# Kernel tuning notes

Hardware: AMD Instinct MI355X
Metric: run time of the kernel (lower is better)

## Reference

```python
import jax, jax.numpy as jnp
import numpy as np

# ---- module constants (from GranuleCellLayer.__init__) ----
N_MOSSY = 4096
EXPANSION = 4.0
N_GRANULE = int(N_MOSSY * EXPANSION)  # 16384
SPARSITY = 0.03
K = int(N_GRANULE * SPARSITY)  # 491
DT_MS = 1.0
# ConductanceLIFConfig(v_threshold=-50, v_reset=-65, tau_mem=5, tau_E=2.5, tau_I=6)
V_TH = -50.0
V_RESET = -65.0
TAU_MEM = 5.0
E_LEAK = -65.0   # assumed == v_reset
E_EXC = 0.0      # standard excitatory reversal potential
W_SPARSITY = 0.05  # WeightInitializer.sparse_random sparsity


def setup_inputs() -> dict:
    key = jax.random.key(0)
    k1, k2, k3, k4 = jax.random.split(key, 4)
    mossy_fiber_spikes = (jax.random.uniform(k1, (N_MOSSY,)) < 0.2).astype(jnp.float32)
    # Per-synapse STP efficacy in (0, 1], shape [n_mossy, n_granule].
    mf_efficacy = jax.random.uniform(k2, (N_MOSSY, N_GRANULE), dtype=jnp.float32)
    mask = (jax.random.uniform(k3, (N_GRANULE, N_MOSSY)) < W_SPARSITY).astype(jnp.float32)
    W = mask * jax.random.uniform(k4, (N_GRANULE, N_MOSSY), dtype=jnp.float32)
    return {"mossy_fiber_spikes": mossy_fiber_spikes, "mf_efficacy": mf_efficacy, "W": W}


def _lif_step(g_exc):
    """Single conductance-LIF Euler step from rest (v=v_reset, g_I=0)."""
    v0 = V_RESET
    # dv = dt/tau_mem * ( (E_L - v) + g_E*(E_E - v) )   (no inhibitory input)
    dv = (DT_MS / TAU_MEM) * ((E_LEAK - v0) + g_exc * (E_EXC - v0))
    v = v0 + dv
    return v >= V_TH  # bool spikes [n_granule]


def reference(mossy_fiber_spikes, mf_efficacy, W):
    # effective_weights = W * mf_efficacy.T ; g_exc = effective_weights @ spikes
    g_exc = jnp.einsum('gm,mg,m->g', W, mf_efficacy, mossy_fiber_spikes)  # [n_granule]
    spikes = _lif_step(g_exc)  # bool [n_granule]
    n_spiking = jnp.sum(spikes.astype(jnp.int32))
    # winner-take-all: keep top-k by excitatory conductance among spiking cells
    masked = jnp.where(spikes, g_exc, -jnp.inf)
    _, top_idx = jax.lax.top_k(masked, K)
    sparse_spikes = jnp.zeros((N_GRANULE,), dtype=bool).at[top_idx].set(True)
    out = jnp.where(n_spiking > K, sparse_spikes, spikes)
    return out
```

## Files before the change

### kernel.cpp

```cpp
#include <hip/hip_runtime.h>

#define N_MOSSY   4096
#define N_GRANULE 16384
#define K_TOP     491
#define M_SPLIT   16
#define M_PER     (N_MOSSY / M_SPLIT)
#define G_BLOCKS  (N_GRANULE / 256)

__global__ __launch_bounds__(256) void gexc_partial(
    const float* __restrict__ spikes,
    const float* __restrict__ eff,
    const float* __restrict__ W,
    float* __restrict__ partial)
{
    __shared__ int s_act[M_PER];
    __shared__ int s_cnt[4];
    __shared__ int s_off[5];

    const int tid  = threadIdx.x;
    const int lane = tid & 63;
    const int wv   = tid >> 6;
    const int mb   = blockIdx.x;
    const int gb   = blockIdx.y;
    const int ms   = mb * M_PER;

    const int m    = ms + wv * 64 + lane;
    const bool p   = spikes[m] > 0.0f;
    const unsigned long long mk = __ballot(p);
    const int pre  = __popcll(mk & ((1ull << lane) - 1ull));
    if (lane == 0) s_cnt[wv] = __popcll(mk);
    __syncthreads();
    if (tid == 0) {
        int o = 0;
        for (int c = 0; c < 4; ++c) { s_off[c] = o; o += s_cnt[c]; }
        s_off[4] = o;
    }
    __syncthreads();
    if (p) s_act[s_off[wv] + pre] = m;
    __syncthreads();
    const int nact = s_off[4];

    const int g = gb * 256 + tid;
    const float* __restrict__ wrow = W + (size_t)g * N_MOSSY;

    float acc = 0.0f;
    int j = 0;
    for (; j + 4 <= nact; j += 4) {
        const int m0 = s_act[j + 0], m1 = s_act[j + 1];
        const int m2 = s_act[j + 2], m3 = s_act[j + 3];
        const float w0 = wrow[m0], w1 = wrow[m1], w2 = wrow[m2], w3 = wrow[m3];
        const float e0 = eff[(size_t)m0 * N_GRANULE + g];
        const float e1 = eff[(size_t)m1 * N_GRANULE + g];
        const float e2 = eff[(size_t)m2 * N_GRANULE + g];
        const float e3 = eff[(size_t)m3 * N_GRANULE + g];
        acc += w0 * e0; acc += w1 * e1; acc += w2 * e2; acc += w3 * e3;
    }
    for (; j < nact; ++j) {
        const int m0 = s_act[j];
        acc += wrow[m0] * eff[(size_t)m0 * N_GRANULE + g];
    }
    partial[(size_t)mb * N_GRANULE + g] = acc;
}

#define NB   2048
#define BIN0 7680
#define CAP  2048

__global__ __launch_bounds__(1024) void reduce_select(
    const float* __restrict__ partial,
    int* __restrict__ out)
{
    __shared__ int s_hist[NB];
    __shared__ int s_scan[1024];
    __shared__ unsigned int s_cbits[CAP];
    __shared__ int s_cidx[CAP];
    __shared__ int s_ccnt;
    __shared__ int s_nspk;
    __shared__ int s_B;
    __shared__ int s_need;

    const int t = threadIdx.x;

    float gx[16];
    #pragma unroll
    for (int i = 0; i < 16; ++i) {
        const int g = i * 1024 + t;
        float a = 0.0f;
        #pragma unroll
        for (int s = 0; s < M_SPLIT; ++s)
            a += partial[(size_t)s * N_GRANULE + g];
        gx[i] = a;
    }

    unsigned int ubits[16];
    int spkmask = 0;
    int myspk = 0;
    #pragma unroll
    for (int i = 0; i < 16; ++i) {
        const float dv = 0.2f * (0.0f + gx[i] * 65.0f);
        const float v  = -65.0f + dv;
        const bool s   = (v >= -50.0f);
        if (s) { spkmask |= (1 << i); ++myspk; }
        ubits[i] = __float_as_uint(gx[i]);
    }

    if (t == 0) { s_ccnt = 0; s_nspk = 0; s_B = -1; s_need = 0; }
    for (int b = t; b < NB; b += 1024) s_hist[b] = 0;
    __syncthreads();

    atomicAdd(&s_nspk, myspk);
    #pragma unroll
    for (int i = 0; i < 16; ++i) {
        if ((spkmask >> i) & 1) {
            int b = (int)(ubits[i] >> 17) - BIN0;
            b = b < 0 ? 0 : (b >= NB ? NB - 1 : b);
            atomicAdd(&s_hist[b], 1);
        }
    }
    __syncthreads();

    const int nspk = s_nspk;

    if (nspk > K_TOP) {
        s_scan[t] = s_hist[2 * t] + s_hist[2 * t + 1];
        __syncthreads();
        for (int off = 1; off < 1024; off <<= 1) {
            const int v = (t + off < 1024) ? s_scan[t + off] : 0;
            __syncthreads();
            s_scan[t] += v;
            __syncthreads();
        }
        const int suf0 = s_scan[t];
        const int suf1 = s_scan[t] - s_hist[2 * t];
        if (suf0 >= K_TOP) atomicMax(&s_B, 2 * t);
        if (suf1 >= K_TOP) atomicMax(&s_B, 2 * t + 1);
        __syncthreads();
        const int B = s_B;
        if (t == 0) {
            const int sufB = s_scan[B >> 1] - ((B & 1) ? s_hist[B & ~1] : 0);
            s_need = K_TOP - (sufB - s_hist[B]);
        }
        __syncthreads();
        const int need = s_need;

        #pragma unroll
        for (int i = 0; i < 16; ++i) {
            if ((spkmask >> i) & 1) {
                int b = (int)(ubits[i] >> 17) - BIN0;
                b = b < 0 ? 0 : (b >= NB ? NB - 1 : b);
                if (b == B) {
                    const int pos = atomicAdd(&s_ccnt, 1);
                    if (pos < CAP) {
                        s_cbits[pos] = ubits[i];
                        s_cidx[pos]  = i * 1024 + t;
                    }
                }
            }
        }
        __syncthreads();
        int C = s_ccnt; if (C > CAP) C = CAP;

        #pragma unroll
        for (int i = 0; i < 16; ++i) {
            const int g = i * 1024 + t;
            bool sel = false;
            if ((spkmask >> i) & 1) {
                int b = (int)(ubits[i] >> 17) - BIN0;
                b = b < 0 ? 0 : (b >= NB ? NB - 1 : b);
                if (b > B) {
                    sel = true;
                } else if (b == B) {
                    int rank = 0;
                    for (int j = 0; j < C; ++j) {
                        const unsigned int cb = s_cbits[j];
                        const int ci = s_cidx[j];
                        if (cb > ubits[i] || (cb == ubits[i] && ci < g)) ++rank;
                    }
                    sel = (rank < need);
                }
            }
            out[g] = sel ? 1 : 0;
        }
    } else {
        #pragma unroll
        for (int i = 0; i < 16; ++i) {
            const int g = i * 1024 + t;
            out[g] = ((spkmask >> i) & 1) ? 1 : 0;
        }
    }
}

extern "C" void kernel_launch(void* const* d_in, const int* in_sizes, int n_in,
                              void* d_out, int out_size, void* d_ws, size_t ws_size,
                              hipStream_t stream) {
    const float* spikes = (const float*)d_in[0];
    const float* eff    = (const float*)d_in[1];
    const float* W      = (const float*)d_in[2];
    int* out       = (int*)d_out;
    float* partial = (float*)d_ws;

    gexc_partial<<<dim3(M_SPLIT, G_BLOCKS), 256, 0, stream>>>(spikes, eff, W, partial);
    reduce_select<<<1, 1024, 0, stream>>>(partial, out);
}
```

Measured before the change: 588.4 us.

## Stage W tiles via coalesced LDS transpose and parallelize reduction across blocks

After: 524.4 us. 1.12x faster.

```diff
diff --git a/kernel.cpp b/kernel.cpp
--- a/kernel.cpp
+++ b/kernel.cpp
@@ -4,15 +4,30 @@
 #define N_GRANULE 16384
 #define K_TOP     491
 #define M_SPLIT   16
-#define M_PER     (N_MOSSY / M_SPLIT)
-#define G_BLOCKS  (N_GRANULE / 256)
+#define M_PER     256
+#define G_BLOCKS  64
+#define CH        32
+#define NCH       (M_PER / CH)
+#define LDS_PAD   257
+
+#define NB   2048
+#define BIN0 7680
+#define CAP  2048
+
+#define WS_PARTIAL 0
+#define WS_UBITS   (M_SPLIT * N_GRANULE)
+#define WS_HIST    (WS_UBITS + N_GRANULE)
+#define WS_NSPK    (WS_HIST + NB)
 
 __global__ __launch_bounds__(256) void gexc_partial(
     const float* __restrict__ spikes,
     const float* __restrict__ eff,
     const float* __restrict__ W,
-    float* __restrict__ partial)
+    float* __restrict__ partial,
+    int* __restrict__ hist,
+    int* __restrict__ nspk)
 {
+    __shared__ float wl[CH][LDS_PAD];
     __shared__ int s_act[M_PER];
     __shared__ int s_cnt[4];
     __shared__ int s_off[5];
@@ -24,8 +39,13 @@
     const int gb   = blockIdx.y;
     const int ms   = mb * M_PER;
 
-    const int m    = ms + wv * 64 + lane;
-    const bool p   = spikes[m] > 0.0f;
+    if (mb == 0) {
+        if (gb < 8) hist[gb * 256 + tid] = 0;
+        else if (gb == 8 && tid == 0) *nspk = 0;
+    }
+
+    const int m0   = ms + wv * 64 + lane;
+    const bool p   = spikes[m0] > 0.0f;
     const unsigned long long mk = __ballot(p);
     const int pre  = __popcll(mk & ((1ull << lane) - 1ull));
     if (lane == 0) s_cnt[wv] = __popcll(mk);
@@ -36,38 +56,68 @@
         s_off[4] = o;
     }
     __syncthreads();
-    if (p) s_act[s_off[wv] + pre] = m;
+    if (p) s_act[s_off[wv] + pre] = m0;
     __syncthreads();
     const int nact = s_off[4];
 
     const int g = gb * 256 + tid;
-    const float* __restrict__ wrow = W + (size_t)g * N_MOSSY;
 
     float acc = 0.0f;
     int j = 0;
-    for (; j + 4 <= nact; j += 4) {
-        const int m0 = s_act[j + 0], m1 = s_act[j + 1];
-        const int m2 = s_act[j + 2], m3 = s_act[j + 3];
-        const float w0 = wrow[m0], w1 = wrow[m1], w2 = wrow[m2], w3 = wrow[m3];
-        const float e0 = eff[(size_t)m0 * N_GRANULE + g];
-        const float e1 = eff[(size_t)m1 * N_GRANULE + g];
-        const float e2 = eff[(size_t)m2 * N_GRANULE + g];
-        const float e3 = eff[(size_t)m3 * N_GRANULE + g];
-        acc += w0 * e0; acc += w1 * e1; acc += w2 * e2; acc += w3 * e3;
-    }
-    for (; j < nact; ++j) {
-        const int m0 = s_act[j];
-        acc += wrow[m0] * eff[(size_t)m0 * N_GRANULE + g];
+    for (int c = 0; c < NCH; ++c) {
+        #pragma unroll
+        for (int i = 0; i < 8; ++i) {
+            const int f  = i * 256 + tid;
+            const int gl = f >> 3;
+            const int m4 = f & 7;
+            const float4 v = *reinterpret_cast<const float4*>(
+                &W[(size_t)(gb * 256 + gl) * N_MOSSY + ms + c * CH + m4 * 4]);
+            wl[m4 * 4 + 0][gl] = v.x;
+            wl[m4 * 4 + 1][gl] = v.y;
+            wl[m4 * 4 + 2][gl] = v.z;
+            wl[m4 * 4 + 3][gl] = v.w;
+        }
+        __syncthreads();
+        const int cend = ms + (c + 1) * CH;
+        const int cbase = ms + c * CH;
+        while (j < nact && s_act[j] < cend) {
+            const int m = s_act[j];
+            acc += wl[m - cbase][tid] * eff[(size_t)m * N_GRANULE + g];
+            ++j;
+        }
+        __syncthreads();
     }
     partial[(size_t)mb * N_GRANULE + g] = acc;
 }
 
-#define NB   2048
-#define BIN0 7680
-#define CAP  2048
-
-__global__ __launch_bounds__(1024) void reduce_select(
+__global__ __launch_bounds__(1024) void reduce_lif(
     const float* __restrict__ partial,
+    unsigned int* __restrict__ ubits,
+    int* __restrict__ hist,
+    int* __restrict__ nspk)
+{
+    const int g = blockIdx.x * 1024 + threadIdx.x;
+    float a = 0.0f;
+    #pragma unroll
+    for (int s = 0; s < M_SPLIT; ++s)
+        a += partial[(size_t)s * N_GRANULE + g];
+    const unsigned int ub = __float_as_uint(a);
+    ubits[g] = ub;
+    const float v = -65.0f + 0.2f * (0.0f + a * 65.0f);
+    const bool sp = (v >= -50.0f);
+    const unsigned long long mk = __ballot(sp);
+    if ((threadIdx.x & 63) == 0) atomicAdd(nspk, __popcll(mk));
+    if (sp) {
+        int b = (int)(ub >> 17) - BIN0;
+        b = b < 0 ? 0 : (b >= NB ? NB - 1 : b);
+        atomicAdd(&hist[b], 1);
+    }
+}
+
+__global__ __launch_bounds__(1024) void select_topk(
+    const unsigned int* __restrict__ ubits,
+    const int* __restrict__ hist,
+    const int* __restrict__ nspk,
     int* __restrict__ out)
 {
     __shared__ int s_hist[NB];
@@ -75,53 +125,28 @@
     __shared__ unsigned int s_cbits[CAP];
     __shared__ int s_cidx[CAP];
     __shared__ int s_ccnt;
-    __shared__ int s_nspk;
     __shared__ int s_B;
     __shared__ int s_need;
 
     const int t = threadIdx.x;
 
-    float gx[16];
+    unsigned int u[16];
+    int spkmask = 0;
     #pragma unroll
     for (int i = 0; i < 16; ++i) {
-        const int g = i * 1024 + t;
-        float a = 0.0f;
-        #pragma unroll
-        for (int s = 0; s < M_SPLIT; ++s)
-            a += partial[(size_t)s * N_GRANULE + g];
-        gx[i] = a;
-    }
-
-    unsigned int ubits[16];
-    int spkmask = 0;
-    int myspk = 0;
-    #pragma unroll
-    for (int i = 0; i < 16; ++i) {
-        const float dv = 0.2f * (0.0f + gx[i] * 65.0f);
-        const float v  = -65.0f + dv;
-        const bool s   = (v >= -50.0f);
-        if (s) { spkmask |= (1 << i); ++myspk; }
-        ubits[i] = __float_as_uint(gx[i]);
-    }
-
-    if (t == 0) { s_ccnt = 0; s_nspk = 0; s_B = -1; s_need = 0; }
-    for (int b = t; b < NB; b += 1024) s_hist[b] = 0;
-    __syncthreads();
-
-    atomicAdd(&s_nspk, myspk);
-    #pragma unroll
-    for (int i = 0; i < 16; ++i) {
-        if ((spkmask >> i) & 1) {
-            int b = (int)(ubits[i] >> 17) - BIN0;
-            b = b < 0 ? 0 : (b >= NB ? NB - 1 : b);
-            atomicAdd(&s_hist[b], 1);
-        }
-    }
-    __syncthreads();
-
-    const int nspk = s_nspk;
-
-    if (nspk > K_TOP) {
+        u[i] = ubits[i * 1024 + t];
+        const float a = __uint_as_float(u[i]);
+        const float v = -65.0f + 0.2f * (0.0f + a * 65.0f);
+        if (v >= -50.0f) spkmask |= (1 << i);
+    }
+    s_hist[t] = hist[t];
+    s_hist[t + 1024] = hist[t + 1024];
+    if (t == 0) { s_ccnt = 0; s_B = -1; s_need = 0; }
+    __syncthreads();
+
+    const int ns = *nspk;
+
+    if (ns > K_TOP) {
         s_scan[t] = s_hist[2 * t] + s_hist[2 * t + 1];
         __syncthreads();
         for (int off = 1; off < 1024; off <<= 1) {
@@ -146,12 +171,12 @@
         #pragma unroll
         for (int i = 0; i < 16; ++i) {
             if ((spkmask >> i) & 1) {
-                int b = (int)(ubits[i] >> 17) - BIN0;
+                int b = (int)(u[i] >> 17) - BIN0;
                 b = b < 0 ? 0 : (b >= NB ? NB - 1 : b);
                 if (b == B) {
                     const int pos = atomicAdd(&s_ccnt, 1);
                     if (pos < CAP) {
-                        s_cbits[pos] = ubits[i];
+                        s_cbits[pos] = u[i];
                         s_cidx[pos]  = i * 1024 + t;
                     }
                 }
@@ -165,16 +190,16 @@
             const int g = i * 1024 + t;
             bool sel = false;
             if ((spkmask >> i) & 1) {
-                int b = (int)(ubits[i] >> 17) - BIN0;
+                int b = (int)(u[i] >> 17) - BIN0;
                 b = b < 0 ? 0 : (b >= NB ? NB - 1 : b);
                 if (b > B) {
                     sel = true;
                 } else if (b == B) {
                     int rank = 0;
-                    for (int j = 0; j < C; ++j) {
-                        const unsigned int cb = s_cbits[j];
-                        const int ci = s_cidx[j];
-                        if (cb > ubits[i] || (cb == ubits[i] && ci < g)) ++rank;
+                    for (int jj = 0; jj < C; ++jj) {
+                        const unsigned int cb = s_cbits[jj];
+                        const int ci = s_cidx[jj];
+                        if (cb > u[i] || (cb == u[i] && ci < g)) ++rank;
                     }
                     sel = (rank < need);
                 }
@@ -196,9 +221,15 @@
     const float* spikes = (const float*)d_in[0];
     const float* eff    = (const float*)d_in[1];
     const float* W      = (const float*)d_in[2];
-    int* out       = (int*)d_out;
-    float* partial = (float*)d_ws;
-
-    gexc_partial<<<dim3(M_SPLIT, G_BLOCKS), 256, 0, stream>>>(spikes, eff, W, partial);
-    reduce_select<<<1, 1024, 0, stream>>>(partial, out);
-}
+    int* out = (int*)d_out;
+
+    float*        partial = (float*)d_ws + WS_PARTIAL;
+    unsigned int* ubits   = (unsigned int*)d_ws + WS_UBITS;
+    int*          hist    = (int*)d_ws + WS_HIST;
+    int*          nspk    = (int*)d_ws + WS_NSPK;
+
+    gexc_partial<<<dim3(M_SPLIT, G_BLOCKS), 256, 0, stream>>>(spikes, eff, W,
+                                                              partial, hist, nspk);
+    reduce_lif<<<M_SPLIT, 1024, 0, stream>>>(partial, ubits, hist, nspk);
+    select_topk<<<1, 1024, 0, stream>>>(ubits, hist, nspk, out);
+}
```
